# Performance work log

Measured on AMD Instinct MI355X. Metric: run time of the kernel, lower is better.

Reference implementation:

```python
import jax, jax.numpy as jnp
import numpy as np

MARGIN = 0.1  # init kwarg


def setup_inputs() -> dict:
    key = jax.random.key(0)
    k1, k2, k3 = jax.random.split(key, 3)
    B, P, D = 256, 64, 1024
    imFtr = jax.random.normal(k1, (B, P, D), dtype=jnp.float32)
    disFtr = jax.random.normal(k2, (B, D), dtype=jnp.float32)
    lblList = jax.random.randint(k3, (B,), 0, 100000, dtype=jnp.int64 if jax.config.read('jax_enable_x64') else jnp.int32)
    return {"imFtr": imFtr, "disFtr": disFtr, "lblList": lblList}


def reference(imFtr, disFtr, lblList):
    B, P, D = imFtr.shape
    # simMM: [B*P, B] -> [B, P, B]; max over proposals P -> simMax [B, B]
    simMM = jnp.einsum('bpd,cd->bpc', imFtr, disFtr)
    simMax = jnp.max(simMM, axis=1)  # [B, B] (rows: image/video i, cols: text j)
    pos = jnp.diagonal(simMax)       # [B]

    # valid negative pairs: labels differ (diagonal excluded automatically)
    mask = (lblList[:, None] != lblList[None, :]).astype(simMax.dtype)  # [B, B]
    pairNum = jnp.sum(mask)

    # image -> text ranking: relu(sim[i, j] - sim[i, i] + margin)
    loss_it = jnp.sum(jnp.maximum(simMax - pos[:, None] + MARGIN, 0.0) * mask)
    loss = loss_it / pairNum

    # biLossFlag: text -> image ranking: relu(sim[j, i] - sim[i, i] + margin)
    loss_ti = jnp.sum(jnp.maximum(simMax - pos[None, :] + MARGIN, 0.0) * mask)
    loss = loss + jnp.where(pairNum > 0, loss_ti / pairNum, 0.0)

    return loss.reshape(1)
```

## Files before the change

### kernel.cpp

```cpp
#include <hip/hip_runtime.h>

constexpr int NB = 256;
constexpr int NP = 64;
constexpr int ND = 1024;
constexpr float MARGIN = 0.1f;

typedef __attribute__((ext_vector_type(8))) short bf16x8;
typedef __attribute__((ext_vector_type(4))) short bf16x4;
typedef __attribute__((ext_vector_type(4))) float f32x4;

static __device__ inline unsigned short f2bf(float f) {
  unsigned u = __builtin_bit_cast(unsigned, f);
  u += 0x7fffu + ((u >> 16) & 1u);
  return (unsigned short)(u >> 16);
}

static __device__ inline bf16x8 cvt8(float4 a, float4 b) {
  bf16x8 r;
  r[0] = (short)f2bf(a.x); r[1] = (short)f2bf(a.y);
  r[2] = (short)f2bf(a.z); r[3] = (short)f2bf(a.w);
  r[4] = (short)f2bf(b.x); r[5] = (short)f2bf(b.y);
  r[6] = (short)f2bf(b.z); r[7] = (short)f2bf(b.w);
  return r;
}

static __device__ inline bf16x4 cvt4(float4 a) {
  bf16x4 r;
  r[0] = (short)f2bf(a.x); r[1] = (short)f2bf(a.y);
  r[2] = (short)f2bf(a.z); r[3] = (short)f2bf(a.w);
  return r;
}

__global__ __launch_bounds__(256) void cvtB_kernel(
    const float* __restrict__ src, short* __restrict__ dst) {
  const int idx = (blockIdx.x * 256 + threadIdx.x) * 4;
  float4 v = *reinterpret_cast<const float4*>(src + idx);
  *reinterpret_cast<bf16x4*>(dst + idx) = cvt4(v);
}

__global__ __launch_bounds__(512) void simmax_kernel(
    const float* __restrict__ imFtr, const short* __restrict__ disB,
    float* __restrict__ simMax) {
  const int i  = blockIdx.x;
  const int t  = threadIdx.x;
  const int w  = t >> 6;
  const int l  = t & 63;
  const int lr = l & 15;
  const int lk = l >> 4;
  const int r7 = lr & 7;

  __shared__ short Asl[2][NP][256];

  f32x4 acc[4][2];
#pragma unroll
  for (int pt = 0; pt < 4; ++pt)
#pragma unroll
    for (int ct = 0; ct < 2; ++ct)
#pragma unroll
      for (int r = 0; r < 4; ++r) acc[pt][ct][r] = 0.0f;

  const int ar  = t >> 3;
  const int aj  = t & 7;
  const int ar7 = ar & 7;
  const float* abase = imFtr + ((size_t)i * NP + ar) * ND + aj * 4;

  const short* bp0 = disB + (size_t)(w * 32 + lr) * ND + lk * 8;
  const short* bp1 = bp0 + (size_t)16 * ND;

  bf16x8 bfr[4][2], bnx[4][2];
  float4 areg[8];

#define LOAD_B(DST, KC)                                                      \
  _Pragma("unroll")                                                          \
  for (int kk = 0; kk < 4; ++kk) {                                           \
    DST[kk][0] = *reinterpret_cast<const bf16x8*>(bp0 + ((KC) + kk) * 32);   \
    DST[kk][1] = *reinterpret_cast<const bf16x8*>(bp1 + ((KC) + kk) * 32);   \
  }

#define STAGE_LOAD(C)                                                        \
  _Pragma("unroll")                                                          \
  for (int g = 0; g < 8; ++g)                                                \
    areg[g] = *reinterpret_cast<const float4*>(abase + (C) * 256 + g * 32);

#define STAGE_WRITE(BUF)                                                     \
  _Pragma("unroll")                                                          \
  for (int g = 0; g < 8; ++g) {                                              \
    const int Gl = g * 4 + (aj >> 1);                                        \
    const int sl = (Gl ^ ar7) * 8 + (aj & 1) * 4;                            \
    *reinterpret_cast<bf16x4*>(&Asl[BUF][ar][sl]) = cvt4(areg[g]);           \
  }

#define COMPUTE_QUARTER(BQ, GBASE)                                           \
  _Pragma("unroll")                                                          \
  for (int kk = 0; kk < 4; ++kk) {                                           \
    const int sl = (((GBASE) + kk * 4 + lk) ^ r7) * 8;                       \
    bf16x8 a0 = *reinterpret_cast<const bf16x8*>(&Asl[cb][lr][sl]);          \
    bf16x8 a1 = *reinterpret_cast<const bf16x8*>(&Asl[cb][16 + lr][sl]);     \
    bf16x8 a2 = *reinterpret_cast<const bf16x8*>(&Asl[cb][32 + lr][sl]);     \
    bf16x8 a3 = *reinterpret_cast<const bf16x8*>(&Asl[cb][48 + lr][sl]);     \
    acc[0][0] = __builtin_amdgcn_mfma_f32_16x16x32_bf16(a0, BQ[kk][0], acc[0][0], 0, 0, 0); \
    acc[0][1] = __builtin_amdgcn_mfma_f32_16x16x32_bf16(a0, BQ[kk][1], acc[0][1], 0, 0, 0); \
    acc[1][0] = __builtin_amdgcn_mfma_f32_16x16x32_bf16(a1, BQ[kk][0], acc[1][0], 0, 0, 0); \
    acc[1][1] = __builtin_amdgcn_mfma_f32_16x16x32_bf16(a1, BQ[kk][1], acc[1][1], 0, 0, 0); \
    acc[2][0] = __builtin_amdgcn_mfma_f32_16x16x32_bf16(a2, BQ[kk][0], acc[2][0], 0, 0, 0); \
    acc[2][1] = __builtin_amdgcn_mfma_f32_16x16x32_bf16(a2, BQ[kk][1], acc[2][1], 0, 0, 0); \
    acc[3][0] = __builtin_amdgcn_mfma_f32_16x16x32_bf16(a3, BQ[kk][0], acc[3][0], 0, 0, 0); \
    acc[3][1] = __builtin_amdgcn_mfma_f32_16x16x32_bf16(a3, BQ[kk][1], acc[3][1], 0, 0, 0); \
  }

  LOAD_B(bfr, 0);
  STAGE_LOAD(0);
  STAGE_WRITE(0);
  __syncthreads();

#pragma unroll
  for (int c = 0; c < 4; ++c) {
    const int cb = c & 1;
    LOAD_B(bnx, c * 8 + 4);
    if (c < 3) STAGE_LOAD(c + 1);
    COMPUTE_QUARTER(bfr, 0);
    if (c < 3) LOAD_B(bfr, (c + 1) * 8);
    COMPUTE_QUARTER(bnx, 16);
    if (c < 3) {
      STAGE_WRITE(cb ^ 1);
      __syncthreads();
    }
  }

#undef LOAD_B
#undef STAGE_LOAD
#undef STAGE_WRITE
#undef COMPUTE_QUARTER

#pragma unroll
  for (int ct = 0; ct < 2; ++ct) {
    float m = acc[0][ct][0];
#pragma unroll
    for (int pt = 0; pt < 4; ++pt)
#pragma unroll
      for (int r = 0; r < 4; ++r) m = fmaxf(m, acc[pt][ct][r]);
    m = fmaxf(m, __shfl_xor(m, 16));
    m = fmaxf(m, __shfl_xor(m, 32));
    if (l < 16) simMax[(size_t)i * NB + w * 32 + ct * 16 + lr] = m;
  }
}

__global__ __launch_bounds__(512) void simmax_fallback_kernel(
    const float* __restrict__ imFtr, const float* __restrict__ disFtr,
    float* __restrict__ simMax) {
  const int i  = blockIdx.x;
  const int t  = threadIdx.x;
  const int w  = t >> 6;
  const int l  = t & 63;
  const int lr = l & 15;
  const int lk = l >> 4;

  __shared__ short Asl[NP][64];

  f32x4 acc[4][2];
#pragma unroll
  for (int pt = 0; pt < 4; ++pt)
#pragma unroll
    for (int ct = 0; ct < 2; ++ct)
#pragma unroll
      for (int r = 0; r < 4; ++r) acc[pt][ct][r] = 0.0f;

  const int ar  = t >> 3;
  const int aks = t & 7;
  const float* ap = imFtr + (size_t)i * NP * ND + (size_t)ar * ND + aks * 8;
  const int wslot = ((aks ^ (ar & 7)) * 8);
  float4 av0 = *reinterpret_cast<const float4*>(ap);
  float4 av1 = *reinterpret_cast<const float4*>(ap + 4);

  const float* bp0 = disFtr + (size_t)(w * 32 + lr) * ND + lk * 8;
  const float* bp1 = disFtr + (size_t)(w * 32 + 16 + lr) * ND + lk * 8;

  for (int kc = 0; kc < 16; ++kc) {
    const int kbase = kc * 64;
    float4 bld[2][2][2];
#pragma unroll
    for (int ks = 0; ks < 2; ++ks) {
      const int ko = kbase + ks * 32;
      bld[ks][0][0] = *reinterpret_cast<const float4*>(bp0 + ko);
      bld[ks][0][1] = *reinterpret_cast<const float4*>(bp0 + ko + 4);
      bld[ks][1][0] = *reinterpret_cast<const float4*>(bp1 + ko);
      bld[ks][1][1] = *reinterpret_cast<const float4*>(bp1 + ko + 4);
    }
    __syncthreads();
    *reinterpret_cast<bf16x8*>(&Asl[ar][wslot]) = cvt8(av0, av1);
    if (kc < 15) {
      const float* apn = ap + (kc + 1) * 64;
      av0 = *reinterpret_cast<const float4*>(apn);
      av1 = *reinterpret_cast<const float4*>(apn + 4);
    }
    __syncthreads();

#pragma unroll
    for (int ks = 0; ks < 2; ++ks) {
      bf16x8 bfr0 = cvt8(bld[ks][0][0], bld[ks][0][1]);
      bf16x8 bfr1 = cvt8(bld[ks][1][0], bld[ks][1][1]);
#pragma unroll
      for (int pt = 0; pt < 4; ++pt) {
        const int row  = pt * 16 + lr;
        const int slot = (((ks * 4 + lk) ^ (row & 7)) * 8);
        bf16x8 afr = *reinterpret_cast<const bf16x8*>(&Asl[row][slot]);
        acc[pt][0] = __builtin_amdgcn_mfma_f32_16x16x32_bf16(afr, bfr0, acc[pt][0], 0, 0, 0);
        acc[pt][1] = __builtin_amdgcn_mfma_f32_16x16x32_bf16(afr, bfr1, acc[pt][1], 0, 0, 0);
      }
    }
  }

#pragma unroll
  for (int ct = 0; ct < 2; ++ct) {
    float m = acc[0][ct][0];
#pragma unroll
    for (int pt = 0; pt < 4; ++pt)
#pragma unroll
      for (int r = 0; r < 4; ++r) m = fmaxf(m, acc[pt][ct][r]);
    m = fmaxf(m, __shfl_xor(m, 16));
    m = fmaxf(m, __shfl_xor(m, 32));
    if (l < 16) simMax[(size_t)i * NB + w * 32 + ct * 16 + l] = m;
  }
}

__global__ __launch_bounds__(256) void loss_kernel(
    const float* __restrict__ simMax, const int* __restrict__ lbl,
    float* __restrict__ partial) {
  const int i = blockIdx.x;
  const int j = threadIdx.x;
  __shared__ float posi_sh;
  __shared__ float red[3][4];

  float s = simMax[(size_t)i * NB + j];
  if (j == i) posi_sh = s;
  __syncthreads();
  const float posi = posi_sh;
  const float posj = simMax[(size_t)j * NB + j];

  const float msk = (lbl[i] != lbl[j]) ? 1.0f : 0.0f;
  float c  = msk;
  float l1 = msk * fmaxf(s - posi + MARGIN, 0.0f);
  float l2 = msk * fmaxf(s - posj + MARGIN, 0.0f);
#pragma unroll
  for (int o = 32; o > 0; o >>= 1) {
    c  += __shfl_down(c, o);
    l1 += __shfl_down(l1, o);
    l2 += __shfl_down(l2, o);
  }
  const int w = j >> 6;
  if ((j & 63) == 0) { red[0][w] = c; red[1][w] = l1; red[2][w] = l2; }
  __syncthreads();
  if (j == 0) {
    partial[i * 3 + 0] = red[0][0] + red[0][1] + red[0][2] + red[0][3];
    partial[i * 3 + 1] = red[1][0] + red[1][1] + red[1][2] + red[1][3];
    partial[i * 3 + 2] = red[2][0] + red[2][1] + red[2][2] + red[2][3];
  }
}

__global__ __launch_bounds__(256) void finalize_kernel(
    const float* __restrict__ partial, float* __restrict__ out) {
  const int t = threadIdx.x;
  __shared__ float red[3][4];
  float c  = partial[t * 3 + 0];
  float l1 = partial[t * 3 + 1];
  float l2 = partial[t * 3 + 2];
#pragma unroll
  for (int o = 32; o > 0; o >>= 1) {
    c  += __shfl_down(c, o);
    l1 += __shfl_down(l1, o);
    l2 += __shfl_down(l2, o);
  }
  const int w = t >> 6;
  if ((t & 63) == 0) { red[0][w] = c; red[1][w] = l1; red[2][w] = l2; }
  __syncthreads();
  if (t == 0) {
    float cs  = red[0][0] + red[0][1] + red[0][2] + red[0][3];
    float l1s = red[1][0] + red[1][1] + red[1][2] + red[1][3];
    float l2s = red[2][0] + red[2][1] + red[2][2] + red[2][3];
    float loss = l1s / cs;
    loss += (cs > 0.0f) ? (l2s / cs) : 0.0f;
    out[0] = loss;
  }
}

extern "C" void kernel_launch(void* const* d_in, const int* in_sizes, int n_in,
                              void* d_out, int out_size, void* d_ws, size_t ws_size,
                              hipStream_t stream) {
  (void)in_sizes; (void)n_in; (void)out_size;
  const float* imFtr  = (const float*)d_in[0];
  const float* disFtr = (const float*)d_in[1];
  const int*   lbl    = (const int*)d_in[2];
  float* out = (float*)d_out;

  const size_t disB_bytes = (size_t)NB * ND * sizeof(short);
  const size_t sim_bytes  = (size_t)NB * NB * sizeof(float);
  const size_t need = disB_bytes + sim_bytes + 3 * NB * sizeof(float);

  if (ws_size >= need) {
    short* disB    = (short*)d_ws;
    float* simMax  = (float*)((char*)d_ws + disB_bytes);
    float* partial = (float*)((char*)d_ws + disB_bytes + sim_bytes);

    cvtB_kernel<<<dim3(NB), dim3(256), 0, stream>>>(disFtr, disB);
    simmax_kernel<<<dim3(NB), dim3(512), 0, stream>>>(imFtr, disB, simMax);
    loss_kernel<<<dim3(NB), dim3(256), 0, stream>>>(simMax, lbl, partial);
    finalize_kernel<<<dim3(1), dim3(256), 0, stream>>>(partial, out);
  } else {
    float* simMax  = (float*)d_ws;
    float* partial = (float*)((char*)d_ws + (size_t)NB * NB * 4);
    simmax_fallback_kernel<<<dim3(NB), dim3(512), 0, stream>>>(imFtr, disFtr, simMax);
    loss_kernel<<<dim3(NB), dim3(256), 0, stream>>>(simMax, lbl, partial);
    finalize_kernel<<<dim3(1), dim3(256), 0, stream>>>(partial, out);
  }
}
```

Before: 36.62 us.

## Use 16 waves per block with one 16-column tile each in simmax

```diff
diff --git a/kernel.cpp b/kernel.cpp
--- a/kernel.cpp
+++ b/kernel.cpp
@@ -38,7 +38,7 @@
   *reinterpret_cast<bf16x4*>(dst + idx) = cvt4(v);
 }
 
-__global__ __launch_bounds__(512) void simmax_kernel(
+__global__ __launch_bounds__(1024, 4) void simmax_kernel(
     const float* __restrict__ imFtr, const short* __restrict__ disB,
     float* __restrict__ simMax) {
   const int i  = blockIdx.x;
@@ -47,102 +47,79 @@
   const int l  = t & 63;
   const int lr = l & 15;
   const int lk = l >> 4;
-  const int r7 = lr & 7;
 
   __shared__ short Asl[2][NP][256];
 
-  f32x4 acc[4][2];
+  f32x4 acc[4];
 #pragma unroll
   for (int pt = 0; pt < 4; ++pt)
 #pragma unroll
-    for (int ct = 0; ct < 2; ++ct)
-#pragma unroll
-      for (int r = 0; r < 4; ++r) acc[pt][ct][r] = 0.0f;
-
-  const int ar  = t >> 3;
-  const int aj  = t & 7;
-  const int ar7 = ar & 7;
+    for (int r = 0; r < 4; ++r) acc[pt][r] = 0.0f;
+
+  const int ar = t >> 4;
+  const int aj = t & 15;
   const float* abase = imFtr + ((size_t)i * NP + ar) * ND + aj * 4;
-
-  const short* bp0 = disB + (size_t)(w * 32 + lr) * ND + lk * 8;
-  const short* bp1 = bp0 + (size_t)16 * ND;
-
-  bf16x8 bfr[4][2], bnx[4][2];
-  float4 areg[8];
-
-#define LOAD_B(DST, KC)                                                      \
-  _Pragma("unroll")                                                          \
-  for (int kk = 0; kk < 4; ++kk) {                                           \
-    DST[kk][0] = *reinterpret_cast<const bf16x8*>(bp0 + ((KC) + kk) * 32);   \
-    DST[kk][1] = *reinterpret_cast<const bf16x8*>(bp1 + ((KC) + kk) * 32);   \
-  }
+  float4 areg[4];
+
+  const short* bp = disB + (size_t)(w * 16 + lr) * ND + lk * 8;
+  bf16x8 breg[8];
 
 #define STAGE_LOAD(C)                                                        \
   _Pragma("unroll")                                                          \
-  for (int g = 0; g < 8; ++g)                                                \
-    areg[g] = *reinterpret_cast<const float4*>(abase + (C) * 256 + g * 32);
+  for (int g = 0; g < 4; ++g)                                                \
+    areg[g] = *reinterpret_cast<const float4*>(abase + (C) * 256 + g * 64);
 
 #define STAGE_WRITE(BUF)                                                     \
   _Pragma("unroll")                                                          \
-  for (int g = 0; g < 8; ++g) {                                              \
-    const int Gl = g * 4 + (aj >> 1);                                        \
-    const int sl = (Gl ^ ar7) * 8 + (aj & 1) * 4;                            \
-    *reinterpret_cast<bf16x4*>(&Asl[BUF][ar][sl]) = cvt4(areg[g]);           \
-  }
-
-#define COMPUTE_QUARTER(BQ, GBASE)                                           \
-  _Pragma("unroll")                                                          \
-  for (int kk = 0; kk < 4; ++kk) {                                           \
-    const int sl = (((GBASE) + kk * 4 + lk) ^ r7) * 8;                       \
-    bf16x8 a0 = *reinterpret_cast<const bf16x8*>(&Asl[cb][lr][sl]);          \
-    bf16x8 a1 = *reinterpret_cast<const bf16x8*>(&Asl[cb][16 + lr][sl]);     \
-    bf16x8 a2 = *reinterpret_cast<const bf16x8*>(&Asl[cb][32 + lr][sl]);     \
-    bf16x8 a3 = *reinterpret_cast<const bf16x8*>(&Asl[cb][48 + lr][sl]);     \
-    acc[0][0] = __builtin_amdgcn_mfma_f32_16x16x32_bf16(a0, BQ[kk][0], acc[0][0], 0, 0, 0); \
-    acc[0][1] = __builtin_amdgcn_mfma_f32_16x16x32_bf16(a0, BQ[kk][1], acc[0][1], 0, 0, 0); \
-    acc[1][0] = __builtin_amdgcn_mfma_f32_16x16x32_bf16(a1, BQ[kk][0], acc[1][0], 0, 0, 0); \
-    acc[1][1] = __builtin_amdgcn_mfma_f32_16x16x32_bf16(a1, BQ[kk][1], acc[1][1], 0, 0, 0); \
-    acc[2][0] = __builtin_amdgcn_mfma_f32_16x16x32_bf16(a2, BQ[kk][0], acc[2][0], 0, 0, 0); \
-    acc[2][1] = __builtin_amdgcn_mfma_f32_16x16x32_bf16(a2, BQ[kk][1], acc[2][1], 0, 0, 0); \
-    acc[3][0] = __builtin_amdgcn_mfma_f32_16x16x32_bf16(a3, BQ[kk][0], acc[3][0], 0, 0, 0); \
-    acc[3][1] = __builtin_amdgcn_mfma_f32_16x16x32_bf16(a3, BQ[kk][1], acc[3][1], 0, 0, 0); \
-  }
-
-  LOAD_B(bfr, 0);
+  for (int g = 0; g < 4; ++g) {                                              \
+    const int s  = g * 8 + (aj >> 1);                                        \
+    const int so = (s ^ (ar & 15)) * 8 + (aj & 1) * 4;                       \
+    *reinterpret_cast<bf16x4*>(&Asl[BUF][ar][so]) = cvt4(areg[g]);           \
+  }
+
   STAGE_LOAD(0);
+#pragma unroll
+  for (int j = 0; j < 8; ++j)
+    breg[j] = *reinterpret_cast<const bf16x8*>(bp + j * 32);
   STAGE_WRITE(0);
   __syncthreads();
 
 #pragma unroll
   for (int c = 0; c < 4; ++c) {
     const int cb = c & 1;
-    LOAD_B(bnx, c * 8 + 4);
     if (c < 3) STAGE_LOAD(c + 1);
-    COMPUTE_QUARTER(bfr, 0);
-    if (c < 3) LOAD_B(bfr, (c + 1) * 8);
-    COMPUTE_QUARTER(bnx, 16);
+#pragma unroll
+    for (int j8 = 0; j8 < 8; ++j8) {
+      const int jj = c * 8 + j8;
+      const int so = ((j8 * 4 + lk) ^ lr) * 8;
+      bf16x8 a0 = *reinterpret_cast<const bf16x8*>(&Asl[cb][lr][so]);
+      bf16x8 a1 = *reinterpret_cast<const bf16x8*>(&Asl[cb][16 + lr][so]);
+      bf16x8 a2 = *reinterpret_cast<const bf16x8*>(&Asl[cb][32 + lr][so]);
+      bf16x8 a3 = *reinterpret_cast<const bf16x8*>(&Asl[cb][48 + lr][so]);
+      acc[0] = __builtin_amdgcn_mfma_f32_16x16x32_bf16(a0, breg[j8], acc[0], 0, 0, 0);
+      acc[1] = __builtin_amdgcn_mfma_f32_16x16x32_bf16(a1, breg[j8], acc[1], 0, 0, 0);
+      acc[2] = __builtin_amdgcn_mfma_f32_16x16x32_bf16(a2, breg[j8], acc[2], 0, 0, 0);
+      acc[3] = __builtin_amdgcn_mfma_f32_16x16x32_bf16(a3, breg[j8], acc[3], 0, 0, 0);
+      if (jj + 8 < 32)
+        breg[j8] = *reinterpret_cast<const bf16x8*>(bp + (jj + 8) * 32);
+    }
     if (c < 3) {
       STAGE_WRITE(cb ^ 1);
       __syncthreads();
     }
   }
 
-#undef LOAD_B
 #undef STAGE_LOAD
 #undef STAGE_WRITE
-#undef COMPUTE_QUARTER
-
-#pragma unroll
-  for (int ct = 0; ct < 2; ++ct) {
-    float m = acc[0][ct][0];
-#pragma unroll
-    for (int pt = 0; pt < 4; ++pt)
-#pragma unroll
-      for (int r = 0; r < 4; ++r) m = fmaxf(m, acc[pt][ct][r]);
-    m = fmaxf(m, __shfl_xor(m, 16));
-    m = fmaxf(m, __shfl_xor(m, 32));
-    if (l < 16) simMax[(size_t)i * NB + w * 32 + ct * 16 + lr] = m;
-  }
+
+  float m = acc[0][0];
+#pragma unroll
+  for (int pt = 0; pt < 4; ++pt)
+#pragma unroll
+    for (int r = 0; r < 4; ++r) m = fmaxf(m, acc[pt][r]);
+  m = fmaxf(m, __shfl_xor(m, 16));
+  m = fmaxf(m, __shfl_xor(m, 32));
+  if (l < 16) simMax[(size_t)i * NB + w * 16 + lr] = m;
 }
 
 __global__ __launch_bounds__(512) void simmax_fallback_kernel(
@@ -302,7 +279,7 @@
     float* partial = (float*)((char*)d_ws + disB_bytes + sim_bytes);
 
     cvtB_kernel<<<dim3(NB), dim3(256), 0, stream>>>(disFtr, disB);
-    simmax_kernel<<<dim3(NB), dim3(512), 0, stream>>>(imFtr, disB, simMax);
+    simmax_kernel<<<dim3(NB), dim3(1024), 0, stream>>>(imFtr, disB, simMax);
     loss_kernel<<<dim3(NB), dim3(256), 0, stream>>>(simMax, lbl, partial);
     finalize_kernel<<<dim3(1), dim3(256), 0, stream>>>(partial, out);
   } else {
```

Measured after the change: 34.48 us. -5.8%, faster.
